# Performance work log

Measured on AMD Instinct MI355X. Metric: run time of the kernel, lower is better.

## Reference

```python
import jax, jax.numpy as jnp
import numpy as np

EMB = 1024
HID = 4096
NHEADS = 16
DK = EMB // NHEADS
EPS = 1e-6
B, S = 2, 2048


def setup_inputs() -> dict:
    key = jax.random.key(0)
    ks = jax.random.split(key, 10)
    sc = 0.02
    return {
        "x": jax.random.normal(ks[0], (B, S, EMB), dtype=jnp.float32),
        "src_mask": jnp.ones((B, 1, 1, S), dtype=jnp.int32),
        "wq": jax.random.normal(ks[1], (EMB, EMB), dtype=jnp.float32) * sc,
        "wk": jax.random.normal(ks[2], (EMB, EMB), dtype=jnp.float32) * sc,
        "wv": jax.random.normal(ks[3], (EMB, EMB), dtype=jnp.float32) * sc,
        "wo": jax.random.normal(ks[4], (EMB, EMB), dtype=jnp.float32) * sc,
        "ff1_w": jax.random.normal(ks[5], (EMB, HID), dtype=jnp.float32) * sc,
        "ff1_b": jnp.zeros((HID,), dtype=jnp.float32),
        "ff2_w": jax.random.normal(ks[6], (HID, EMB), dtype=jnp.float32) * sc,
        "ff2_b": jnp.zeros((EMB,), dtype=jnp.float32),
        "ln1_a": jnp.ones((1,), dtype=jnp.float32),
        "ln1_b": jnp.zeros((1,), dtype=jnp.float32),
        "ln2_a": jnp.ones((1,), dtype=jnp.float32),
        "ln2_b": jnp.zeros((1,), dtype=jnp.float32),
    }


def layernorm(x, alpha, bias):
    # Faithful to the custom LayerNorm: scalar alpha/bias, std with Bessel
    # correction (torch default unbiased=True), divide by (std + eps).
    mean = jnp.mean(x, axis=-1, keepdims=True)
    var = jnp.sum((x - mean) ** 2, axis=-1, keepdims=True) / (x.shape[-1] - 1)
    std = jnp.sqrt(var)
    return alpha * (x - mean) / (std + EPS) + bias


def mha(x, mask, wq, wk, wv, wo):
    b, s, _ = x.shape
    def split_heads(t):  # [B,S,E] -> [B,H,S,dk]
        return t.reshape(b, s, NHEADS, DK).transpose(0, 2, 1, 3)
    q = split_heads(x @ wq)
    k = split_heads(x @ wk)
    v = split_heads(x @ wv)
    scores = jnp.einsum("bhqd,bhkd->bhqk", q, k) / jnp.sqrt(jnp.float32(DK))
    scores = jnp.where(mask == 0, -jnp.inf, scores)
    attn = jax.nn.softmax(scores, axis=-1)
    out = jnp.einsum("bhqk,bhkd->bhqd", attn, v)
    out = out.transpose(0, 2, 1, 3).reshape(b, s, EMB)
    return out @ wo


def ffn(x, w1, b1, w2, b2):
    return jax.nn.relu(x @ w1 + b1) @ w2 + b2


def reference(x, src_mask, wq, wk, wv, wo, ff1_w, ff1_b, ff2_w, ff2_b,
              ln1_a, ln1_b, ln2_a, ln2_b):
    # pre-norm residual encoder block (dropout=0 / eval mode)
    h = x + mha(layernorm(x, ln1_a, ln1_b), src_mask, wq, wk, wv, wo)
    out = h + ffn(layernorm(h, ln2_a, ln2_b), ff1_w, ff1_b, ff2_w, ff2_b)
    return out
```

## Files before the change

kernel.cpp:

```cpp
#include <hip/hip_runtime.h>
#include <stdint.h>

#define EMB 1024
#define HID 4096
#define NHEADS 16
#define DKH 64
#define SEQ 2048
#define BATCH 2
#define MROWS (BATCH * SEQ)
#define GBK 64

typedef unsigned short u16;
typedef __attribute__((ext_vector_type(8))) short short8;
typedef __attribute__((ext_vector_type(4))) float f32x4;

#if __has_builtin(__builtin_amdgcn_exp2f)
#define QK_SCALE 0.18033688011f
#define QK_CLAMP 43.3f
__device__ __forceinline__ float pexp(float x) { return __builtin_amdgcn_exp2f(x); }
#else
#define QK_SCALE 0.125f
#define QK_CLAMP 30.0f
__device__ __forceinline__ float pexp(float x) { return __expf(x); }
#endif

__device__ __forceinline__ float bf2f(u16 h) {
    return __uint_as_float(((unsigned)h) << 16);
}
__device__ __forceinline__ u16 f2bf(float f) {
    unsigned u = __float_as_uint(f);
    unsigned r = 0x7FFFu + ((u >> 16) & 1u);
    return (u16)((u + r) >> 16);
}
__device__ __forceinline__ f32x4 mfma16(short8 a, short8 b, f32x4 c) {
    return __builtin_amdgcn_mfma_f32_16x16x32_bf16(a, b, c, 0, 0, 0);
}
__device__ __forceinline__ void gl_lds16(const u16* g, u16* l) {
    __builtin_amdgcn_global_load_lds(
        (__attribute__((address_space(1))) void*)g,
        (__attribute__((address_space(3))) void*)l, 16, 0, 0);
}

__global__ __launch_bounds__(256) void transpose_qkvo(
    const float* __restrict__ wq, const float* __restrict__ wk,
    const float* __restrict__ wv, const float* __restrict__ wo,
    u16* __restrict__ qkvT, u16* __restrict__ woT) {
    __shared__ u16 t[32][33];
    const int z = blockIdx.z;
    const float* W = (z == 0) ? wq : (z == 1) ? wk : (z == 2) ? wv : wo;
    u16* WT = (z < 3) ? (qkvT + (size_t)z * EMB * EMB) : woT;
    const float scale = (z == 0) ? QK_SCALE : 1.0f;
    const int tx = threadIdx.x & 31, ty = threadIdx.x >> 5;
    const int k0 = blockIdx.y * 32, n0 = blockIdx.x * 32;
#pragma unroll
    for (int r = 0; r < 32; r += 8)
        t[ty + r][tx] = f2bf(scale * W[(size_t)(k0 + ty + r) * EMB + n0 + tx]);
    __syncthreads();
#pragma unroll
    for (int r = 0; r < 32; r += 8)
        WT[(size_t)(n0 + ty + r) * EMB + k0 + tx] = t[tx][ty + r];
}

__global__ __launch_bounds__(256) void transpose_bf16(
    const float* __restrict__ W, u16* __restrict__ WT, int K, int N) {
    __shared__ u16 t[32][33];
    const int tx = threadIdx.x & 31, ty = threadIdx.x >> 5;
    const int k0 = blockIdx.y * 32, n0 = blockIdx.x * 32;
#pragma unroll
    for (int r = 0; r < 32; r += 8)
        t[ty + r][tx] = f2bf(W[(size_t)(k0 + ty + r) * N + n0 + tx]);
    __syncthreads();
#pragma unroll
    for (int r = 0; r < 32; r += 8)
        WT[(size_t)(n0 + ty + r) * K + k0 + tx] = t[tx][ty + r];
}

__global__ __launch_bounds__(256) void ln_kernel(
    const float* __restrict__ x, u16* __restrict__ out,
    const float* __restrict__ alpha_p, const float* __restrict__ beta_p) {
    const int row = blockIdx.x;
    const int tid = threadIdx.x;
    float4 v = reinterpret_cast<const float4*>(x + (size_t)row * EMB)[tid];

    __shared__ float red[4];
    float s = v.x + v.y + v.z + v.w;
    for (int off = 32; off; off >>= 1) s += __shfl_down(s, off);
    if ((tid & 63) == 0) red[tid >> 6] = s;
    __syncthreads();
    float mean = (red[0] + red[1] + red[2] + red[3]) * (1.0f / EMB);
    __syncthreads();

    float d0 = v.x - mean, d1 = v.y - mean, d2 = v.z - mean, d3 = v.w - mean;
    float sq = d0 * d0 + d1 * d1 + d2 * d2 + d3 * d3;
    for (int off = 32; off; off >>= 1) sq += __shfl_down(sq, off);
    if ((tid & 63) == 0) red[tid >> 6] = sq;
    __syncthreads();
    float var = (red[0] + red[1] + red[2] + red[3]) * (1.0f / (EMB - 1));
    float inv = 1.0f / (sqrtf(var) + 1e-6f);
    float a = alpha_p[0], b = beta_p[0];

    ushort4 o;
    o.x = f2bf(a * d0 * inv + b);
    o.y = f2bf(a * d1 * inv + b);
    o.z = f2bf(a * d2 * inv + b);
    o.w = f2bf(a * d3 * inv + b);
    reinterpret_cast<ushort4*>(out + (size_t)row * EMB)[tid] = o;
}

template <int BN, int NWM>
__global__ __launch_bounds__(256) void gemm_mfma(
    const u16* __restrict__ A, const u16* __restrict__ BT, void* C,
    const float* __restrict__ bias, const void* res,
    int M, int N, int K, int relu, int out_mode,
    u16* __restrict__ Kb_out, u16* __restrict__ VT_out) {
    constexpr int NWN = 4 / NWM;
    constexpr int WM = 128 / (16 * NWM);
    constexpr int WN = BN / (16 * NWN);
    __shared__ u16 As[128][GBK];
    __shared__ u16 Bs[BN][GBK];

    const int tid = threadIdx.x;
    const int wave = tid >> 6, lane = tid & 63;
    const int quad = lane >> 4, lc = lane & 15;
    const int wm = wave % NWM, wn = wave / NWM;

    const int nx = gridDim.x;
    const int bid = blockIdx.y * nx + blockIdx.x;
    const int xcd = bid & 7, sl = bid >> 3;
    const int nyx = gridDim.y >> 3;
    const int bcol = sl % nx;
    const int brow = (sl / nx) + xcd * nyx;
    const int row0 = brow * 128, col0 = bcol * BN;

    const int srow = lane >> 3;
    const int scg = (lane & 7) ^ srow;

    f32x4 acc[WM][WN] = {};

    for (int k0 = 0; k0 < K; k0 += GBK) {
        __syncthreads();
#pragma unroll
        for (int i = 0; i < 4; ++i) {
            const int rb = wave * 32 + i * 8;
            gl_lds16(A + (size_t)(row0 + rb + srow) * K + k0 + scg * 8, &As[rb][0]);
        }
#pragma unroll
        for (int i = 0; i < BN / 32; ++i) {
            const int rb = wave * (BN / 4) + i * 8;
            gl_lds16(BT + (size_t)(col0 + rb + srow) * K + k0 + scg * 8, &Bs[rb][0]);
        }
        __syncthreads();

#pragma unroll
        for (int s = 0; s < 2; ++s) {
            short8 af[WM], bfv[WN];
#pragma unroll
            for (int i = 0; i < WM; ++i) {
                const int ar = wm * (16 * WM) + i * 16 + lc;
                af[i] = *reinterpret_cast<const short8*>(
                    &As[ar][(((s * 4 + quad) ^ (ar & 7))) * 8]);
            }
#pragma unroll
            for (int j = 0; j < WN; ++j) {
                const int br = wn * (16 * WN) + j * 16 + lc;
                bfv[j] = *reinterpret_cast<const short8*>(
                    &Bs[br][(((s * 4 + quad) ^ (br & 7))) * 8]);
            }
#pragma unroll
            for (int i = 0; i < WM; ++i)
#pragma unroll
                for (int j = 0; j < WN; ++j)
                    acc[i][j] = mfma16(af[i], bfv[j], acc[i][j]);
        }
    }

    u16* Cb = (u16*)C;
    int mode = out_mode, ncols = N, lcol0 = col0;
    if (out_mode == 3) {
        const int seg = col0 >> 10;
        lcol0 = col0 & 1023;
        ncols = EMB;
        if (seg == 1) { Cb = Kb_out; mode = 0; }
        else if (seg == 2) { Cb = VT_out; mode = 2; }
        else { mode = 0; }
    }

#pragma unroll
    for (int j = 0; j < WN; ++j) {
        const int col = lcol0 + wn * (16 * WN) + j * 16 + lc;
        const float bv = bias ? bias[col] : 0.f;
#pragma unroll
        for (int i = 0; i < WM; ++i) {
            const int rbase = row0 + wm * (16 * WM) + i * 16 + quad * 4;
            if (mode == 2) {
                ushort4 o;
                o.x = f2bf(acc[i][j][0]); o.y = f2bf(acc[i][j][1]);
                o.z = f2bf(acc[i][j][2]); o.w = f2bf(acc[i][j][3]);
                *reinterpret_cast<ushort4*>(Cb + (size_t)col * M + rbase) = o;
            } else {
#pragma unroll
                for (int r = 0; r < 4; ++r) {
                    const size_t idx = (size_t)(rbase + r) * ncols + col;
                    float v = acc[i][j][r] + bv;
                    if (relu) v = fmaxf(v, 0.f);
                    if (res) v += ((const float*)res)[idx];
                    if (mode == 1) ((float*)C)[idx] = v;
                    else Cb[idx] = f2bf(v);
                }
            }
        }
    }
}

__global__ __launch_bounds__(256) void attn_mfma(
    const u16* __restrict__ Q, const u16* __restrict__ K,
    const u16* __restrict__ VT, const int* __restrict__ mask,
    u16* __restrict__ O) {
    const int tid = threadIdx.x;
    const int wave = tid >> 6, lane = tid & 63;
    const int quad = lane >> 4, lc = lane & 15;
    const int H = blockIdx.x & 31;
    const int qblk = blockIdx.x >> 5;
    const int h = H & 15, b = H >> 4;
    const int q0 = qblk * 64 + wave * 16;

    __shared__ u16 Ks[64][64];
    __shared__ u16 Vs[64][64];
    __shared__ u16 Pl[4][16][64];

    const u16* qbase = Q + (size_t)(b * SEQ + q0 + lc) * EMB + h * DKH + quad * 8;
    const short8 qb0 = *reinterpret_cast<const short8*>(qbase);
    const short8 qb1 = *reinterpret_cast<const short8*>(qbase + 32);

    const int srow = lane >> 3;
    const int scg = (lane & 7) ^ srow;

    f32x4 o[4] = {};
    float rs = 0.f;

    for (int kc = 0; kc < SEQ; kc += 64) {
        __syncthreads();
        if (wave < 2) {
#pragma unroll
            for (int i = 0; i < 4; ++i) {
                const int r = wave * 32 + i * 8;
                gl_lds16(K + (size_t)(b * SEQ + kc + r + srow) * EMB + h * DKH + scg * 8,
                         &Ks[r][0]);
            }
        } else {
#pragma unroll
            for (int i = 0; i < 4; ++i) {
                const int d = (wave - 2) * 32 + i * 8;
                gl_lds16(VT + (size_t)(h * DKH + d + srow) * MROWS + b * SEQ + kc + scg * 8,
                         &Vs[d][0]);
            }
        }
        __syncthreads();

#pragma unroll
        for (int t = 0; t < 4; ++t) {
            const int krow = t * 16 + lc;
            const short8 ka0 = *reinterpret_cast<const short8*>(
                &Ks[krow][(quad ^ (krow & 7)) * 8]);
            const short8 ka1 = *reinterpret_cast<const short8*>(
                &Ks[krow][((4 + quad) ^ (krow & 7)) * 8]);
            f32x4 st = {};
            st = mfma16(ka0, qb0, st);
            st = mfma16(ka1, qb1, st);
            const int4 mk = *reinterpret_cast<const int4*>(
                mask + b * SEQ + kc + t * 16 + quad * 4);
            const int* mkp = &mk.x;
            unsigned up[4];
#pragma unroll
            for (int r = 0; r < 4; ++r) {
                float p = pexp(fminf(st[r], QK_CLAMP));
                p = mkp[r] ? p : 0.f;
                rs += p;
                up[r] = __float_as_uint(p);
            }
            uint2 pw;
            pw.x = __builtin_amdgcn_perm(up[1], up[0], 0x07060302u);
            pw.y = __builtin_amdgcn_perm(up[3], up[2], 0x07060302u);
            const int kg = (t * 2 + (quad >> 1)) ^ (lc & 7);
            *reinterpret_cast<uint2*>(&Pl[wave][lc][kg * 8 + (quad & 1) * 4]) = pw;
        }

#pragma unroll
        for (int ss = 0; ss < 2; ++ss) {
            const short8 pa = *reinterpret_cast<const short8*>(
                &Pl[wave][lc][((ss * 4 + quad) ^ (lc & 7)) * 8]);
#pragma unroll
            for (int d = 0; d < 4; ++d) {
                const int vrow = d * 16 + lc;
                const short8 vb = *reinterpret_cast<const short8*>(
                    &Vs[vrow][((ss * 4 + quad) ^ (vrow & 7)) * 8]);
                o[d] = mfma16(pa, vb, o[d]);
            }
        }
    }

    float lt = rs;
    lt += __shfl_xor(lt, 16);
    lt += __shfl_xor(lt, 32);
    float lrow[4];
#pragma unroll
    for (int r = 0; r < 4; ++r) lrow[r] = __shfl(lt, quad * 4 + r);

#pragma unroll
    for (int d = 0; d < 4; ++d)
#pragma unroll
        for (int r = 0; r < 4; ++r) {
            const int qrow = quad * 4 + r;
            O[(size_t)(b * SEQ + q0 + qrow) * EMB + h * DKH + d * 16 + lc] =
                f2bf(o[d][r] / lrow[r]);
        }
}

extern "C" void kernel_launch(void* const* d_in, const int* in_sizes, int n_in,
                              void* d_out, int out_size, void* d_ws, size_t ws_size,
                              hipStream_t stream) {
    const float* x     = (const float*)d_in[0];
    const int*   mask  = (const int*)d_in[1];
    const float* wq    = (const float*)d_in[2];
    const float* wk    = (const float*)d_in[3];
    const float* wv    = (const float*)d_in[4];
    const float* wo    = (const float*)d_in[5];
    const float* ff1_w = (const float*)d_in[6];
    const float* ff1_b = (const float*)d_in[7];
    const float* ff2_w = (const float*)d_in[8];
    const float* ff2_b = (const float*)d_in[9];
    const float* ln1_a = (const float*)d_in[10];
    const float* ln1_b = (const float*)d_in[11];
    const float* ln2_a = (const float*)d_in[12];
    const float* ln2_b = (const float*)d_in[13];
    float* out = (float*)d_out;

    char* ws = (char*)d_ws;
    const size_t MB = 1u << 20;
    u16* act   = (u16*)(ws + 0);
    u16* Qb    = (u16*)(ws + 8 * MB);
    u16* Kb    = (u16*)(ws + 16 * MB);
    u16* VTb   = (u16*)(ws + 24 * MB);
    u16* f1    = (u16*)(ws + 8 * MB);
    u16* wqkvT = (u16*)(ws + 40 * MB);
    u16* woT   = (u16*)(ws + 46 * MB);
    u16* ffT   = (u16*)(ws + 40 * MB);

    transpose_qkvo<<<dim3(EMB / 32, EMB / 32, 4), 256, 0, stream>>>(
        wq, wk, wv, wo, wqkvT, woT);

    ln_kernel<<<MROWS, 256, 0, stream>>>(x, act, ln1_a, ln1_b);

    gemm_mfma<128, 2><<<dim3(3 * EMB / 128, MROWS / 128), 256, 0, stream>>>(
        act, wqkvT, Qb, nullptr, nullptr, MROWS, 3 * EMB, EMB, 0, 3, Kb, VTb);

    attn_mfma<<<BATCH * NHEADS * (SEQ / 64), 256, 0, stream>>>(Qb, Kb, VTb, mask, act);

    gemm_mfma<64, 4><<<dim3(EMB / 64, MROWS / 128), 256, 0, stream>>>(
        act, woT, out, nullptr, x, MROWS, EMB, EMB, 0, 1, nullptr, nullptr);

    ln_kernel<<<MROWS, 256, 0, stream>>>(out, act, ln2_a, ln2_b);

    transpose_bf16<<<dim3(HID / 32, EMB / 32), 256, 0, stream>>>(ff1_w, ffT, EMB, HID);
    gemm_mfma<128, 2><<<dim3(HID / 128, MROWS / 128), 256, 0, stream>>>(
        act, ffT, f1, ff1_b, nullptr, MROWS, HID, EMB, 1, 0, nullptr, nullptr);

    transpose_bf16<<<dim3(EMB / 32, HID / 32), 256, 0, stream>>>(ff2_w, ffT, HID, EMB);
    gemm_mfma<64, 4><<<dim3(EMB / 64, MROWS / 128), 256, 0, stream>>>(
        f1, ffT, out, ff2_b, out, MROWS, EMB, HID, 0, 1, nullptr, nullptr);
}
```

Baseline: 390.7 us.

## Double-buffer LDS tiles and use 512-thread blocks in GEMM and attention

The GEMM and attention kernels now keep two LDS buffers and prefetch the next K-tile while computing on the current one, so each loop iteration needs one barrier instead of two. Both kernels move from 4 to 8 waves per block. The GEMM gives each wave a smaller sub-tile, and attention covers 128 queries per block. The goal is to hide global-to-LDS load latency and raise the number of waves in flight. The cost is twice the LDS per block and fewer blocks for attention, which may reduce how many blocks fit per CU.

```diff
diff --git a/kernel.cpp b/kernel.cpp
--- a/kernel.cpp
+++ b/kernel.cpp
@@ -108,16 +108,16 @@
 }
 
 template <int BN, int NWM>
-__global__ __launch_bounds__(256) void gemm_mfma(
+__global__ __launch_bounds__(512) void gemm_mfma(
     const u16* __restrict__ A, const u16* __restrict__ BT, void* C,
     const float* __restrict__ bias, const void* res,
     int M, int N, int K, int relu, int out_mode,
     u16* __restrict__ Kb_out, u16* __restrict__ VT_out) {
-    constexpr int NWN = 4 / NWM;
+    constexpr int NWN = 8 / NWM;
     constexpr int WM = 128 / (16 * NWM);
     constexpr int WN = BN / (16 * NWN);
-    __shared__ u16 As[128][GBK];
-    __shared__ u16 Bs[BN][GBK];
+    __shared__ u16 As[2][128][GBK];
+    __shared__ u16 Bs[2][BN][GBK];
 
     const int tid = threadIdx.x;
     const int wave = tid >> 6, lane = tid & 63;
@@ -137,19 +137,33 @@
 
     f32x4 acc[WM][WN] = {};
 
+    auto stage = [&](int k0, int buf) {
+#pragma unroll
+        for (int i = 0; i < 2; ++i) {
+            const int rb = wave * 16 + i * 8;
+            gl_lds16(A + (size_t)(row0 + rb + srow) * K + k0 + scg * 8,
+                     &As[buf][rb][0]);
+        }
+        if constexpr (BN == 128) {
+#pragma unroll
+            for (int i = 0; i < 2; ++i) {
+                const int rb = wave * 16 + i * 8;
+                gl_lds16(BT + (size_t)(col0 + rb + srow) * K + k0 + scg * 8,
+                         &Bs[buf][rb][0]);
+            }
+        } else {
+            const int rb = wave * 8;
+            gl_lds16(BT + (size_t)(col0 + rb + srow) * K + k0 + scg * 8,
+                     &Bs[buf][rb][0]);
+        }
+    };
+
+    stage(0, 0);
+    __syncthreads();
+    int cur = 0;
+
     for (int k0 = 0; k0 < K; k0 += GBK) {
-        __syncthreads();
-#pragma unroll
-        for (int i = 0; i < 4; ++i) {
-            const int rb = wave * 32 + i * 8;
-            gl_lds16(A + (size_t)(row0 + rb + srow) * K + k0 + scg * 8, &As[rb][0]);
-        }
-#pragma unroll
-        for (int i = 0; i < BN / 32; ++i) {
-            const int rb = wave * (BN / 4) + i * 8;
-            gl_lds16(BT + (size_t)(col0 + rb + srow) * K + k0 + scg * 8, &Bs[rb][0]);
-        }
-        __syncthreads();
+        if (k0 + GBK < K) stage(k0 + GBK, cur ^ 1);
 
 #pragma unroll
         for (int s = 0; s < 2; ++s) {
@@ -158,13 +172,13 @@
             for (int i = 0; i < WM; ++i) {
                 const int ar = wm * (16 * WM) + i * 16 + lc;
                 af[i] = *reinterpret_cast<const short8*>(
-                    &As[ar][(((s * 4 + quad) ^ (ar & 7))) * 8]);
+                    &As[cur][ar][(((s * 4 + quad) ^ (ar & 7))) * 8]);
             }
 #pragma unroll
             for (int j = 0; j < WN; ++j) {
                 const int br = wn * (16 * WN) + j * 16 + lc;
                 bfv[j] = *reinterpret_cast<const short8*>(
-                    &Bs[br][(((s * 4 + quad) ^ (br & 7))) * 8]);
+                    &Bs[cur][br][(((s * 4 + quad) ^ (br & 7))) * 8]);
             }
 #pragma unroll
             for (int i = 0; i < WM; ++i)
@@ -172,6 +186,8 @@
                 for (int j = 0; j < WN; ++j)
                     acc[i][j] = mfma16(af[i], bfv[j], acc[i][j]);
         }
+        __syncthreads();
+        cur ^= 1;
     }
 
     u16* Cb = (u16*)C;
@@ -212,7 +228,7 @@
     }
 }
 
-__global__ __launch_bounds__(256) void attn_mfma(
+__global__ __launch_bounds__(512) void attn_mfma(
     const u16* __restrict__ Q, const u16* __restrict__ K,
     const u16* __restrict__ VT, const int* __restrict__ mask,
     u16* __restrict__ O) {
@@ -222,11 +238,11 @@
     const int H = blockIdx.x & 31;
     const int qblk = blockIdx.x >> 5;
     const int h = H & 15, b = H >> 4;
-    const int q0 = qblk * 64 + wave * 16;
-
-    __shared__ u16 Ks[64][64];
-    __shared__ u16 Vs[64][64];
-    __shared__ u16 Pl[4][16][64];
+    const int q0 = qblk * 128 + wave * 16;
+
+    __shared__ u16 Ks[2][64][64];
+    __shared__ u16 Vs[2][64][64];
+    __shared__ u16 Pl[8][16][64];
 
     const u16* qbase = Q + (size_t)(b * SEQ + q0 + lc) * EMB + h * DKH + quad * 8;
     const short8 qb0 = *reinterpret_cast<const short8*>(qbase);
@@ -235,35 +251,41 @@
     const int srow = lane >> 3;
     const int scg = (lane & 7) ^ srow;
 
+    auto stage = [&](int kc, int buf) {
+        if (wave < 4) {
+#pragma unroll
+            for (int i = 0; i < 2; ++i) {
+                const int r = wave * 16 + i * 8;
+                gl_lds16(K + (size_t)(b * SEQ + kc + r + srow) * EMB + h * DKH + scg * 8,
+                         &Ks[buf][r][0]);
+            }
+        } else {
+#pragma unroll
+            for (int i = 0; i < 2; ++i) {
+                const int d = (wave - 4) * 16 + i * 8;
+                gl_lds16(VT + (size_t)(h * DKH + d + srow) * MROWS + b * SEQ + kc + scg * 8,
+                         &Vs[buf][d][0]);
+            }
+        }
+    };
+
     f32x4 o[4] = {};
     float rs = 0.f;
 
+    stage(0, 0);
+    __syncthreads();
+    int cur = 0;
+
     for (int kc = 0; kc < SEQ; kc += 64) {
-        __syncthreads();
-        if (wave < 2) {
-#pragma unroll
-            for (int i = 0; i < 4; ++i) {
-                const int r = wave * 32 + i * 8;
-                gl_lds16(K + (size_t)(b * SEQ + kc + r + srow) * EMB + h * DKH + scg * 8,
-                         &Ks[r][0]);
-            }
-        } else {
-#pragma unroll
-            for (int i = 0; i < 4; ++i) {
-                const int d = (wave - 2) * 32 + i * 8;
-                gl_lds16(VT + (size_t)(h * DKH + d + srow) * MROWS + b * SEQ + kc + scg * 8,
-                         &Vs[d][0]);
-            }
-        }
-        __syncthreads();
+        if (kc + 64 < SEQ) stage(kc + 64, cur ^ 1);
 
 #pragma unroll
         for (int t = 0; t < 4; ++t) {
             const int krow = t * 16 + lc;
             const short8 ka0 = *reinterpret_cast<const short8*>(
-                &Ks[krow][(quad ^ (krow & 7)) * 8]);
+                &Ks[cur][krow][(quad ^ (krow & 7)) * 8]);
             const short8 ka1 = *reinterpret_cast<const short8*>(
-                &Ks[krow][((4 + quad) ^ (krow & 7)) * 8]);
+                &Ks[cur][krow][((4 + quad) ^ (krow & 7)) * 8]);
             f32x4 st = {};
             st = mfma16(ka0, qb0, st);
             st = mfma16(ka1, qb1, st);
@@ -293,10 +315,12 @@
             for (int d = 0; d < 4; ++d) {
                 const int vrow = d * 16 + lc;
                 const short8 vb = *reinterpret_cast<const short8*>(
-                    &Vs[vrow][((ss * 4 + quad) ^ (vrow & 7)) * 8]);
+                    &Vs[cur][vrow][((ss * 4 + quad) ^ (vrow & 7)) * 8]);
                 o[d] = mfma16(pa, vb, o[d]);
             }
         }
+        __syncthreads();
+        cur ^= 1;
     }
 
     float lt = rs;
@@ -351,21 +375,21 @@
 
     ln_kernel<<<MROWS, 256, 0, stream>>>(x, act, ln1_a, ln1_b);
 
-    gemm_mfma<128, 2><<<dim3(3 * EMB / 128, MROWS / 128), 256, 0, stream>>>(
+    gemm_mfma<128, 2><<<dim3(3 * EMB / 128, MROWS / 128), 512, 0, stream>>>(
         act, wqkvT, Qb, nullptr, nullptr, MROWS, 3 * EMB, EMB, 0, 3, Kb, VTb);
 
-    attn_mfma<<<BATCH * NHEADS * (SEQ / 64), 256, 0, stream>>>(Qb, Kb, VTb, mask, act);
-
-    gemm_mfma<64, 4><<<dim3(EMB / 64, MROWS / 128), 256, 0, stream>>>(
+    attn_mfma<<<BATCH * NHEADS * (SEQ / 128), 512, 0, stream>>>(Qb, Kb, VTb, mask, act);
+
+    gemm_mfma<64, 4><<<dim3(EMB / 64, MROWS / 128), 512, 0, stream>>>(
         act, woT, out, nullptr, x, MROWS, EMB, EMB, 0, 1, nullptr, nullptr);
 
     ln_kernel<<<MROWS, 256, 0, stream>>>(out, act, ln2_a, ln2_b);
 
     transpose_bf16<<<dim3(HID / 32, EMB / 32), 256, 0, stream>>>(ff1_w, ffT, EMB, HID);
-    gemm_mfma<128, 2><<<dim3(HID / 128, MROWS / 128), 256, 0, stream>>>(
+    gemm_mfma<128, 2><<<dim3(HID / 128, MROWS / 128), 512, 0, stream>>>(
         act, ffT, f1, ff1_b, nullptr, MROWS, HID, EMB, 1, 0, nullptr, nullptr);
 
     transpose_bf16<<<dim3(EMB / 32, HID / 32), 256, 0, stream>>>(ff2_w, ffT, HID, EMB);
-    gemm_mfma<64, 4><<<dim3(EMB / 64, MROWS / 128), 256, 0, stream>>>(
+    gemm_mfma<64, 4><<<dim3(EMB / 64, MROWS / 128), 512, 0, stream>>>(
         f1, ffT, out, ff2_b, out, MROWS, EMB, HID, 0, 1, nullptr, nullptr);
 }
```

Result: faster. 371.7 us (-4.9%).
